# Kernel optimization log

Hardware: AMD Instinct MI355X
Metric: run time of the kernel (lower is better)

## Reference

```python
import jax, jax.numpy as jnp
from jax import lax
import numpy as np

B, T, D, H = 2048, 512, 16, 48


def _lstm_layer(x, W_ih, W_hh, b_ih, b_hh):
    """Single-layer LSTM, batch_first. x: [B,T,Din] -> hs: [B,T,H].
    PyTorch gate order: i, f, g, o."""
    h_dim = W_hh.shape[1]
    # Precompute input contribution for all timesteps: [B,T,4H]
    xg = jnp.einsum('btd,gd->btg', x, W_ih) + b_ih + b_hh
    xg = jnp.swapaxes(xg, 0, 1)  # [T,B,4H]

    def step(carry, xg_t):
        h, c = carry
        gates = xg_t + h @ W_hh.T  # [B,4H]
        i, f, g, o = jnp.split(gates, 4, axis=-1)
        i = jax.nn.sigmoid(i)
        f = jax.nn.sigmoid(f)
        g = jnp.tanh(g)
        o = jax.nn.sigmoid(o)
        c = f * c + i * g
        h = o * jnp.tanh(c)
        return (h, c), h

    bsz = x.shape[0]
    init = (jnp.zeros((bsz, h_dim), x.dtype), jnp.zeros((bsz, h_dim), x.dtype))
    _, hs = lax.scan(step, init, xg)
    return jnp.swapaxes(hs, 0, 1)  # [B,T,H]


def setup_inputs() -> dict:
    key = jax.random.key(0)
    ks = jax.random.split(key, 11)
    s_in = 1.0 / np.sqrt(H)
    return {
        'x': jax.random.normal(ks[0], (B, T, D), jnp.float32),
        'W_ih0': jax.random.normal(ks[1], (4 * H, D), jnp.float32) * s_in,
        'W_hh0': jax.random.normal(ks[2], (4 * H, H), jnp.float32) * s_in,
        'b_ih0': jax.random.normal(ks[3], (4 * H,), jnp.float32) * s_in,
        'b_hh0': jax.random.normal(ks[4], (4 * H,), jnp.float32) * s_in,
        'W_ih1': jax.random.normal(ks[5], (4 * H, H), jnp.float32) * s_in,
        'W_hh1': jax.random.normal(ks[6], (4 * H, H), jnp.float32) * s_in,
        'b_ih1': jax.random.normal(ks[7], (4 * H,), jnp.float32) * s_in,
        'b_hh1': jax.random.normal(ks[8], (4 * H,), jnp.float32) * s_in,
        'fc_w': jax.random.normal(ks[9], (1, H), jnp.float32) * s_in,
        'fc_b': jax.random.normal(ks[10], (1,), jnp.float32) * s_in,
    }


def reference(x, W_ih0, W_hh0, b_ih0, b_hh0, W_ih1, W_hh1, b_ih1, b_hh1, fc_w, fc_b):
    # 2-layer LSTM (eval mode: inter-layer dropout is identity)
    h1 = _lstm_layer(x, W_ih0, W_hh0, b_ih0, b_hh0)   # [B,T,H]
    h2 = _lstm_layer(h1, W_ih1, W_hh1, b_ih1, b_hh1)  # [B,T,H]
    last = h2[:, -1, :]                               # [B,H]
    logits = last @ fc_w.T + fc_b                     # [B,1]
    return jax.nn.sigmoid(logits)
```

## Files before the change

### kernel.cpp

```cpp
#include <hip/hip_runtime.h>

#define TT 512
#define DD 16
#define HH 48
#define BT 8
#define NTHR 768
#define CHUNK 64

#define XB 8192
#define STOT (XB + 1536)

typedef short bf8v __attribute__((ext_vector_type(8)));
typedef float f32x4 __attribute__((ext_vector_type(4)));

__device__ __forceinline__ ushort bfb(float f) {
    return __builtin_bit_cast(ushort, (__bf16)f);
}

__device__ __forceinline__ float sigf(float x) {
    float e = __builtin_amdgcn_exp2f(-1.4426950408889634f * x);
    return __builtin_amdgcn_rcpf(1.0f + e);
}

__device__ __forceinline__ void barrier_lds() {
    asm volatile("s_waitcnt lgkmcnt(0)\ns_barrier" ::: "memory");
}

__global__ __launch_bounds__(NTHR)
void lstm_kernel(const float* __restrict__ x,
                 const float* __restrict__ Wih0, const float* __restrict__ Whh0,
                 const float* __restrict__ bih0, const float* __restrict__ bhh0,
                 const float* __restrict__ Wih1, const float* __restrict__ Whh1,
                 const float* __restrict__ bih1, const float* __restrict__ bhh1,
                 const float* __restrict__ fcw, const float* __restrict__ fcb,
                 float* __restrict__ out)
{
    __shared__ alignas(16) ushort S[STOT];
    __shared__ float outl[BT][HH];

    const int tid  = threadIdx.x;
    const int lane = tid & 63;
    const int wave = tid >> 6;
    const int b0   = blockIdx.x * BT;

    const int colq = lane & 15;
    const int quad = lane >> 4;
    const int b    = colq & 7;
    const bool hi  = (colq >= 8);
    const int u    = wave * 4 + quad;

    const float L2E = 1.4426950408889634f;

    const int fbm = b * 8;
    const bool ringlane = (quad >= 2) && !hi;
    const int r0E = XB + quad * 64 + fbm;
    const int r0O = r0E + 768;
    const int r2E = XB + (8 + quad) * 64 + fbm;
    const int r2O = r2E + 768;
    const int r1statE = XB + (4 + quad) * 64 + fbm;
    const int r1statO = r1statE + 768;
    const int r1ring0 = (quad - 2) * 64 + colq * 8;
    const int inc = ringlane ? 256 : 0;
    const int kk = hi ? 48 + u : u;
    const int woff = (kk >> 3) * 64 + b * 8 + (kk & 7);
    const int wE = XB + 768 + woff;
    const int wO = XB + woff;

    f32x4 bias0, bias1;
#pragma unroll
    for (int r = 0; r < 4; ++r) {
        bias0[r] = bih0[r * 48 + u] + bhh0[r * 48 + u];
        bias1[r] = bih1[r * 48 + u] + bhh1[r * 48 + u];
    }

    const int gi = (colq & 3) * 48 + wave * 4 + (colq >> 2);
    bf8v w0k0, w0k1, w1k0, w1k1, w1k2;
    {
        bf8v w;
#pragma unroll
        for (int j = 0; j < 8; ++j) {
            int k = quad * 8 + j;
            w[j] = (short)bfb(Whh0[gi * 48 + k]);
        }
        w0k0 = w;
#pragma unroll
        for (int j = 0; j < 8; ++j) {
            int k = 32 + quad * 8 + j;
            float v = (k < 48) ? Whh0[gi * 48 + k] : Wih0[gi * 16 + (k - 48)];
            w[j] = (short)bfb(v);
        }
        w0k1 = w;
#pragma unroll
        for (int j = 0; j < 8; ++j) {
            int k = quad * 8 + j;
            w[j] = (short)bfb(Wih1[gi * 48 + k]);
        }
        w1k0 = w;
#pragma unroll
        for (int j = 0; j < 8; ++j) {
            int k = 32 + quad * 8 + j;
            float v = (k < 48) ? Wih1[gi * 48 + k] : Whh1[gi * 48 + (k - 48)];
            w[j] = (short)bfb(v);
        }
        w1k1 = w;
#pragma unroll
        for (int j = 0; j < 8; ++j) {
            int k = 64 + quad * 8 + j;
            w[j] = (short)bfb(Whh1[gi * 48 + (k - 48)]);
        }
        w1k2 = w;
    }

    {
        uint* p = (uint*)S;
        for (int i = tid; i < STOT / 2; i += NTHR) p[i] = 0;
    }
    __syncthreads();

    float c = 0.f;
    float hv = 0.f;

#define MFMA(A, B, C) __builtin_amdgcn_mfma_f32_16x16x32_bf16(A, B, C, 0, 0, 0)

#define BODY(V0A, V1A, V2A, WA, DOL1) { \
        bf8v v0 = *(const bf8v*)&S[V0A]; \
        bf8v v1 = *(const bf8v*)&S[V1A]; \
        bf8v v2 = *(const bf8v*)&S[V2A]; \
        f32x4 acc0 = MFMA(w0k0, v0, bias0); \
        acc0 = MFMA(w0k1, v1, acc0); \
        f32x4 pre; \
        if (DOL1) { \
            f32x4 acc1 = MFMA(w1k0, v0, bias1); \
            acc1 = MFMA(w1k1, v1, acc1); \
            acc1 = MFMA(w1k2, v2, acc1); \
            pre[0] = hi ? acc1[0] : acc0[0]; \
            pre[1] = hi ? acc1[1] : acc0[1]; \
            pre[2] = hi ? acc1[2] : acc0[2]; \
            pre[3] = hi ? acc1[3] : acc0[3]; \
        } else { \
            pre = acc0; \
        } \
        float ei = __builtin_amdgcn_exp2f(-L2E * pre[0]); \
        float ef = __builtin_amdgcn_exp2f(-L2E * pre[1]); \
        float eg = __builtin_amdgcn_exp2f(-2.0f * L2E * pre[2]); \
        float eo = __builtin_amdgcn_exp2f(-L2E * pre[3]); \
        float rig = __builtin_amdgcn_rcpf((1.0f + ei) * (1.0f + eg)); \
        float rf  = __builtin_amdgcn_rcpf(1.0f + ef); \
        float cn = __builtin_fmaf(rf, c, (1.0f - eg) * rig); \
        if (!DOL1) cn = hi ? c : cn;    \
        c = cn; \
        float ec = __builtin_amdgcn_exp2f(-2.0f * L2E * cn); \
        float roc = __builtin_amdgcn_rcpf((1.0f + eo) * (1.0f + ec)); \
        hv = (1.0f - ec) * roc; \
        ushort hb = bfb(hv); \
        if (!hi) { S[WA] = hb; } \
        else if (DOL1) { S[WA] = hb; } \
        barrier_lds(); \
    }

    for (int ck = 0; ck < TT / CHUNK; ++ck) {
        for (int i = tid; i < BT * CHUNK * 4; i += NTHR) {
            int g  = i & 3;
            int tl = (i >> 2) & (CHUNK - 1);
            int bb = i >> 8;
            const float4 v = *(const float4*)(x +
                ((size_t)(b0 + bb) * TT + (ck * CHUNK + tl)) * DD + g * 4);
            ushort4 s4;
            s4.x = bfb(v.x); s4.y = bfb(v.y); s4.z = bfb(v.z); s4.w = bfb(v.w);
            *(ushort4*)&S[tl * 128 + (g >> 1) * 64 + bb * 8 + (g & 1) * 4] = s4;
        }
        __syncthreads();

        int r1E = ringlane ? r1ring0 : r1statE;
        int r1O = ringlane ? (128 + r1ring0) : r1statO;

        int p0 = 0;
        if (ck == 0) {
            BODY(r0E, r1E, r2E, wE, false)
            BODY(r0O, r1O, r2O, wO, true)
            r1E += inc; r1O += inc;
            p0 = 1;
        }
        for (int p = p0; p < CHUNK / 2; ++p) {
            BODY(r0E, r1E, r2E, wE, true)
            BODY(r0O, r1O, r2O, wO, true)
            r1E += inc; r1O += inc;
        }
    }

    {
        int r1E = ringlane ? (r1ring0 + 32 * 256) : r1statE;
        bf8v v0 = *(const bf8v*)&S[r0E];
        bf8v v1 = *(const bf8v*)&S[r1E];
        bf8v v2 = *(const bf8v*)&S[r2E];
        f32x4 acc1 = MFMA(w1k0, v0, bias1);
        acc1 = MFMA(w1k1, v1, acc1);
        acc1 = MFMA(w1k2, v2, acc1);
        float ei = __builtin_amdgcn_exp2f(-L2E * acc1[0]);
        float ef = __builtin_amdgcn_exp2f(-L2E * acc1[1]);
        float eg = __builtin_amdgcn_exp2f(-2.0f * L2E * acc1[2]);
        float eo = __builtin_amdgcn_exp2f(-L2E * acc1[3]);
        float rig = __builtin_amdgcn_rcpf((1.0f + ei) * (1.0f + eg));
        float rf  = __builtin_amdgcn_rcpf(1.0f + ef);
        float cn = __builtin_fmaf(rf, c, (1.0f - eg) * rig);
        float ec = __builtin_amdgcn_exp2f(-2.0f * L2E * cn);
        float roc = __builtin_amdgcn_rcpf((1.0f + eo) * (1.0f + ec));
        hv = (1.0f - ec) * roc;
    }

    if (hi) outl[b][u] = hv;
    __syncthreads();
    if (tid < BT) {
        float s = fcb[0];
        for (int uu = 0; uu < HH; ++uu) s = __builtin_fmaf(outl[tid][uu], fcw[uu], s);
        out[b0 + tid] = sigf(s);
    }
#undef BODY
#undef MFMA
}

extern "C" void kernel_launch(void* const* d_in, const int* in_sizes, int n_in,
                              void* d_out, int out_size, void* d_ws, size_t ws_size,
                              hipStream_t stream) {
    const float* x    = (const float*)d_in[0];
    const float* Wih0 = (const float*)d_in[1];
    const float* Whh0 = (const float*)d_in[2];
    const float* bih0 = (const float*)d_in[3];
    const float* bhh0 = (const float*)d_in[4];
    const float* Wih1 = (const float*)d_in[5];
    const float* Whh1 = (const float*)d_in[6];
    const float* bih1 = (const float*)d_in[7];
    const float* bhh1 = (const float*)d_in[8];
    const float* fcw  = (const float*)d_in[9];
    const float* fcb  = (const float*)d_in[10];
    lstm_kernel<<<2048 / BT, NTHR, 0, stream>>>(x, Wih0, Whh0, bih0, bhh0,
                                                Wih1, Whh1, bih1, bhh1, fcw, fcb,
                                                (float*)d_out);
}
```

Baseline: 287.0 us.

## Halve batch tile to 4 rows, two hidden-unit groups per wave, smaller blocks

Result: slower. 374.0 us (+30.3%).

```diff
diff --git a/kernel.cpp b/kernel.cpp
--- a/kernel.cpp
+++ b/kernel.cpp
@@ -3,12 +3,14 @@
 #define TT 512
 #define DD 16
 #define HH 48
-#define BT 8
-#define NTHR 768
+#define BT 4
+#define NTHR 384
 #define CHUNK 64
-
-#define XB 8192
-#define STOT (XB + 1536)
+#define RS 72
+
+#define XB (CHUNK * RS)
+#define PS 384
+#define STOT (XB + 2 * PS)
 
 typedef short bf8v __attribute__((ext_vector_type(8)));
 typedef float f32x4 __attribute__((ext_vector_type(4)));
@@ -26,7 +28,7 @@
     asm volatile("s_waitcnt lgkmcnt(0)\ns_barrier" ::: "memory");
 }
 
-__global__ __launch_bounds__(NTHR)
+__global__ __launch_bounds__(NTHR, 3)
 void lstm_kernel(const float* __restrict__ x,
                  const float* __restrict__ Wih0, const float* __restrict__ Whh0,
                  const float* __restrict__ bih0, const float* __restrict__ bhh0,
@@ -45,71 +47,82 @@
 
     const int colq = lane & 15;
     const int quad = lane >> 4;
-    const int b    = colq & 7;
-    const bool hi  = (colq >= 8);
-    const int u    = wave * 4 + quad;
+    const int b    = colq & 3;
+    const bool Lb  = ((colq >> 2) & 1) != 0;
+    const bool Tq  = (colq >= 8);
+    const int u    = wave * 8 + (Tq ? 4 : 0) + quad;
 
     const float L2E = 1.4426950408889634f;
 
     const int fbm = b * 8;
-    const bool ringlane = (quad >= 2) && !hi;
-    const int r0E = XB + quad * 64 + fbm;
-    const int r0O = r0E + 768;
-    const int r2E = XB + (8 + quad) * 64 + fbm;
-    const int r2O = r2E + 768;
-    const int r1statE = XB + (4 + quad) * 64 + fbm;
-    const int r1statO = r1statE + 768;
-    const int r1ring0 = (quad - 2) * 64 + colq * 8;
-    const int inc = ringlane ? 256 : 0;
-    const int kk = hi ? 48 + u : u;
-    const int woff = (kk >> 3) * 64 + b * 8 + (kk & 7);
-    const int wE = XB + 768 + woff;
+    const bool ringlane = (quad >= 2) && !Lb;
+    const int r0E = XB + quad * 32 + fbm;
+    const int r0O = r0E + PS;
+    const int r1statE = XB + (4 + quad) * 32 + fbm;
+    const int r1statO = r1statE + PS;
+    const int r2E = XB + (8 + quad) * 32 + fbm;
+    const int r2O = r2E + PS;
+    const int r1ring0 = (quad - 2) * 32 + fbm;
+    const int inc = ringlane ? 2 * RS : 0;
+    const int kk = Lb ? 48 + u : u;
+    const int woff = (kk >> 3) * 32 + fbm + (kk & 7);
+    const int wE = XB + PS + woff;
     const int wO = XB + woff;
 
-    f32x4 bias0, bias1;
+    f32x4 bias00, bias01, bias10, bias11;
+    {
+        const int u0 = wave * 8 + quad;
+        const int u1 = u0 + 4;
 #pragma unroll
-    for (int r = 0; r < 4; ++r) {
-        bias0[r] = bih0[r * 48 + u] + bhh0[r * 48 + u];
-        bias1[r] = bih1[r * 48 + u] + bhh1[r * 48 + u];
-    }
-
-    const int gi = (colq & 3) * 48 + wave * 4 + (colq >> 2);
-    bf8v w0k0, w0k1, w1k0, w1k1, w1k2;
-    {
-        bf8v w;
-#pragma unroll
-        for (int j = 0; j < 8; ++j) {
-            int k = quad * 8 + j;
-            w[j] = (short)bfb(Whh0[gi * 48 + k]);
-        }
-        w0k0 = w;
-#pragma unroll
-        for (int j = 0; j < 8; ++j) {
-            int k = 32 + quad * 8 + j;
-            float v = (k < 48) ? Whh0[gi * 48 + k] : Wih0[gi * 16 + (k - 48)];
-            w[j] = (short)bfb(v);
-        }
-        w0k1 = w;
-#pragma unroll
-        for (int j = 0; j < 8; ++j) {
-            int k = quad * 8 + j;
-            w[j] = (short)bfb(Wih1[gi * 48 + k]);
-        }
-        w1k0 = w;
-#pragma unroll
-        for (int j = 0; j < 8; ++j) {
-            int k = 32 + quad * 8 + j;
-            float v = (k < 48) ? Wih1[gi * 48 + k] : Whh1[gi * 48 + (k - 48)];
-            w[j] = (short)bfb(v);
-        }
-        w1k1 = w;
-#pragma unroll
-        for (int j = 0; j < 8; ++j) {
-            int k = 64 + quad * 8 + j;
-            w[j] = (short)bfb(Whh1[gi * 48 + (k - 48)]);
-        }
-        w1k2 = w;
-    }
+        for (int r = 0; r < 4; ++r) {
+            bias00[r] = bih0[r * 48 + u0] + bhh0[r * 48 + u0];
+            bias01[r] = bih0[r * 48 + u1] + bhh0[r * 48 + u1];
+            bias10[r] = bih1[r * 48 + u0] + bhh1[r * 48 + u0];
+            bias11[r] = bih1[r * 48 + u1] + bhh1[r * 48 + u1];
+        }
+    }
+
+    bf8v w0k0_0, w0k1_0, w1k0_0, w1k1_0, w1k2_0;
+    bf8v w0k0_1, w0k1_1, w1k0_1, w1k1_1, w1k2_1;
+#define LOADW(GI, W0K0, W0K1, W1K0, W1K1, W1K2) { \
+        bf8v w; \
+        _Pragma("unroll") \
+        for (int j = 0; j < 8; ++j) {       \
+            w[j] = (short)bfb(Whh0[(GI) * 48 + quad * 8 + j]); \
+        } \
+        W0K0 = w; \
+        _Pragma("unroll") \
+        for (int j = 0; j < 8; ++j) {       \
+            int k = 32 + quad * 8 + j; \
+            float v = (k < 48) ? Whh0[(GI) * 48 + k] : Wih0[(GI) * 16 + (k - 48)]; \
+            w[j] = (short)bfb(v); \
+        } \
+        W0K1 = w; \
+        _Pragma("unroll") \
+        for (int j = 0; j < 8; ++j) {       \
+            w[j] = (short)bfb(Wih1[(GI) * 48 + quad * 8 + j]); \
+        } \
+        W1K0 = w; \
+        _Pragma("unroll") \
+        for (int j = 0; j < 8; ++j) {       \
+            int k = 32 + quad * 8 + j; \
+            float v = (k < 48) ? Wih1[(GI) * 48 + k] : Whh1[(GI) * 48 + (k - 48)]; \
+            w[j] = (short)bfb(v); \
+        } \
+        W1K1 = w; \
+        _Pragma("unroll") \
+        for (int j = 0; j < 8; ++j) {       \
+            w[j] = (short)bfb(Whh1[(GI) * 48 + 16 + quad * 8 + j]); \
+        } \
+        W1K2 = w; \
+    }
+    {
+        const int gi0 = (colq & 3) * 48 + wave * 8 + (colq >> 2);
+        const int gi1 = gi0 + 4;
+        LOADW(gi0, w0k0_0, w0k1_0, w1k0_0, w1k1_0, w1k2_0)
+        LOADW(gi1, w0k0_1, w0k1_1, w1k0_1, w1k1_1, w1k2_1)
+    }
+#undef LOADW
 
     {
         uint* p = (uint*)S;
@@ -126,19 +139,27 @@
         bf8v v0 = *(const bf8v*)&S[V0A]; \
         bf8v v1 = *(const bf8v*)&S[V1A]; \
         bf8v v2 = *(const bf8v*)&S[V2A]; \
-        f32x4 acc0 = MFMA(w0k0, v0, bias0); \
-        acc0 = MFMA(w0k1, v1, acc0); \
+        f32x4 a00 = MFMA(w0k0_0, v0, bias00); \
+        a00 = MFMA(w0k1_0, v1, a00); \
+        f32x4 a01 = MFMA(w0k0_1, v0, bias01); \
+        a01 = MFMA(w0k1_1, v1, a01); \
         f32x4 pre; \
         if (DOL1) { \
-            f32x4 acc1 = MFMA(w1k0, v0, bias1); \
-            acc1 = MFMA(w1k1, v1, acc1); \
-            acc1 = MFMA(w1k2, v2, acc1); \
-            pre[0] = hi ? acc1[0] : acc0[0]; \
-            pre[1] = hi ? acc1[1] : acc0[1]; \
-            pre[2] = hi ? acc1[2] : acc0[2]; \
-            pre[3] = hi ? acc1[3] : acc0[3]; \
+            f32x4 a10 = MFMA(w1k0_0, v0, bias10); \
+            a10 = MFMA(w1k1_0, v1, a10); \
+            a10 = MFMA(w1k2_0, v2, a10); \
+            f32x4 a11 = MFMA(w1k0_1, v0, bias11); \
+            a11 = MFMA(w1k1_1, v1, a11); \
+            a11 = MFMA(w1k2_1, v2, a11); \
+            _Pragma("unroll") \
+            for (int r = 0; r < 4; ++r) { \
+                float l0 = Tq ? a01[r] : a00[r]; \
+                float l1 = Tq ? a11[r] : a10[r]; \
+                pre[r] = Lb ? l1 : l0; \
+            } \
         } else { \
-            pre = acc0; \
+            _Pragma("unroll") \
+            for (int r = 0; r < 4; ++r) pre[r] = Tq ? a01[r] : a00[r]; \
         } \
         float ei = __builtin_amdgcn_exp2f(-L2E * pre[0]); \
         float ef = __builtin_amdgcn_exp2f(-L2E * pre[1]); \
@@ -147,13 +168,13 @@
         float rig = __builtin_amdgcn_rcpf((1.0f + ei) * (1.0f + eg)); \
         float rf  = __builtin_amdgcn_rcpf(1.0f + ef); \
         float cn = __builtin_fmaf(rf, c, (1.0f - eg) * rig); \
-        if (!DOL1) cn = hi ? c : cn;    \
+        if (!DOL1) cn = Lb ? c : cn;    \
         c = cn; \
         float ec = __builtin_amdgcn_exp2f(-2.0f * L2E * cn); \
         float roc = __builtin_amdgcn_rcpf((1.0f + eo) * (1.0f + ec)); \
         hv = (1.0f - ec) * roc; \
         ushort hb = bfb(hv); \
-        if (!hi) { S[WA] = hb; } \
+        if (!Lb) { S[WA] = hb; } \
         else if (DOL1) { S[WA] = hb; } \
         barrier_lds(); \
     }
@@ -167,12 +188,12 @@
                 ((size_t)(b0 + bb) * TT + (ck * CHUNK + tl)) * DD + g * 4);
             ushort4 s4;
             s4.x = bfb(v.x); s4.y = bfb(v.y); s4.z = bfb(v.z); s4.w = bfb(v.w);
-            *(ushort4*)&S[tl * 128 + (g >> 1) * 64 + bb * 8 + (g & 1) * 4] = s4;
+            *(ushort4*)&S[tl * RS + (g >> 1) * 32 + bb * 8 + (g & 1) * 4] = s4;
         }
         __syncthreads();
 
         int r1E = ringlane ? r1ring0 : r1statE;
-        int r1O = ringlane ? (128 + r1ring0) : r1statO;
+        int r1O = ringlane ? (RS + r1ring0) : r1statO;
 
         int p0 = 0;
         if (ck == 0) {
@@ -189,17 +210,22 @@
     }
 
     {
-        int r1E = ringlane ? (r1ring0 + 32 * 256) : r1statE;
         bf8v v0 = *(const bf8v*)&S[r0E];
-        bf8v v1 = *(const bf8v*)&S[r1E];
+        bf8v v1 = *(const bf8v*)&S[r1statE];
         bf8v v2 = *(const bf8v*)&S[r2E];
-        f32x4 acc1 = MFMA(w1k0, v0, bias1);
-        acc1 = MFMA(w1k1, v1, acc1);
-        acc1 = MFMA(w1k2, v2, acc1);
-        float ei = __builtin_amdgcn_exp2f(-L2E * acc1[0]);
-        float ef = __builtin_amdgcn_exp2f(-L2E * acc1[1]);
-        float eg = __builtin_amdgcn_exp2f(-2.0f * L2E * acc1[2]);
-        float eo = __builtin_amdgcn_exp2f(-L2E * acc1[3]);
+        f32x4 a10 = MFMA(w1k0_0, v0, bias10);
+        a10 = MFMA(w1k1_0, v1, a10);
+        a10 = MFMA(w1k2_0, v2, a10);
+        f32x4 a11 = MFMA(w1k0_1, v0, bias11);
+        a11 = MFMA(w1k1_1, v1, a11);
+        a11 = MFMA(w1k2_1, v2, a11);
+        f32x4 pre;
+#pragma unroll
+        for (int r = 0; r < 4; ++r) pre[r] = Tq ? a11[r] : a10[r];
+        float ei = __builtin_amdgcn_exp2f(-L2E * pre[0]);
+        float ef = __builtin_amdgcn_exp2f(-L2E * pre[1]);
+        float eg = __builtin_amdgcn_exp2f(-2.0f * L2E * pre[2]);
+        float eo = __builtin_amdgcn_exp2f(-L2E * pre[3]);
         float rig = __builtin_amdgcn_rcpf((1.0f + ei) * (1.0f + eg));
         float rf  = __builtin_amdgcn_rcpf(1.0f + ef);
         float cn = __builtin_fmaf(rf, c, (1.0f - eg) * rig);
@@ -208,7 +234,7 @@
         hv = (1.0f - ec) * roc;
     }
 
-    if (hi) outl[b][u] = hv;
+    if (Lb) outl[b][u] = hv;
     __syncthreads();
     if (tid < BT) {
         float s = fcb[0];
```

## Prefetch x chunks into registers, fold exp scales into weights, merge reciprocals

Applied to the files above, without the earlier changes.

Measured after the change: 269.5 us. -6.1%, faster.

```diff
diff --git a/kernel.cpp b/kernel.cpp
--- a/kernel.cpp
+++ b/kernel.cpp
@@ -66,11 +66,14 @@
     const int wE = XB + 768 + woff;
     const int wO = XB + woff;
 
+    const float fac = ((colq & 3) == 2) ? (-2.0f * L2E) : (-L2E);
+
     f32x4 bias0, bias1;
 #pragma unroll
     for (int r = 0; r < 4; ++r) {
-        bias0[r] = bih0[r * 48 + u] + bhh0[r * 48 + u];
-        bias1[r] = bih1[r * 48 + u] + bhh1[r * 48 + u];
+        float fr = (r == 2) ? (-2.0f * L2E) : (-L2E);
+        bias0[r] = fr * (bih0[r * 48 + u] + bhh0[r * 48 + u]);
+        bias1[r] = fr * (bih1[r * 48 + u] + bhh1[r * 48 + u]);
     }
 
     const int gi = (colq & 3) * 48 + wave * 4 + (colq >> 2);
@@ -80,35 +83,58 @@
 #pragma unroll
         for (int j = 0; j < 8; ++j) {
             int k = quad * 8 + j;
-            w[j] = (short)bfb(Whh0[gi * 48 + k]);
+            w[j] = (short)bfb(fac * Whh0[gi * 48 + k]);
         }
         w0k0 = w;
 #pragma unroll
         for (int j = 0; j < 8; ++j) {
             int k = 32 + quad * 8 + j;
             float v = (k < 48) ? Whh0[gi * 48 + k] : Wih0[gi * 16 + (k - 48)];
-            w[j] = (short)bfb(v);
+            w[j] = (short)bfb(fac * v);
         }
         w0k1 = w;
 #pragma unroll
         for (int j = 0; j < 8; ++j) {
             int k = quad * 8 + j;
-            w[j] = (short)bfb(Wih1[gi * 48 + k]);
+            w[j] = (short)bfb(fac * Wih1[gi * 48 + k]);
         }
         w1k0 = w;
 #pragma unroll
         for (int j = 0; j < 8; ++j) {
             int k = 32 + quad * 8 + j;
             float v = (k < 48) ? Wih1[gi * 48 + k] : Whh1[gi * 48 + (k - 48)];
-            w[j] = (short)bfb(v);
+            w[j] = (short)bfb(fac * v);
         }
         w1k1 = w;
 #pragma unroll
         for (int j = 0; j < 8; ++j) {
             int k = 64 + quad * 8 + j;
-            w[j] = (short)bfb(Whh1[gi * 48 + (k - 48)]);
+            w[j] = (short)bfb(fac * Whh1[gi * 48 + (k - 48)]);
         }
         w1k2 = w;
+    }
+
+    const int g_  = tid & 3;
+    const int bb_ = (tid >> 2) & 7;
+    const int tlL = tid >> 5;
+    const float* xpA = x + ((size_t)(b0 + bb_) * TT + tlL) * DD + g_ * 4;
+    const float* xpB = xpA + 24 * DD;
+    const int saA = tlL * 128 + (g_ >> 1) * 64 + bb_ * 8 + (g_ & 1) * 4;
+    const int saB = saA + 24 * 128;
+    float4 st0, st1;
+
+#define STAGE(Hn) { \
+        st0 = *(const float4*)(xpA + (Hn) * (32 * DD)); \
+        if (tid < 256) st1 = *(const float4*)(xpB + (Hn) * (32 * DD)); \
+    }
+#define COMMIT(Hn) { \
+        ushort4 s4; \
+        s4.x = bfb(st0.x); s4.y = bfb(st0.y); s4.z = bfb(st0.z); s4.w = bfb(st0.w); \
+        *(ushort4*)&S[saA + ((Hn) & 1) * 4096] = s4; \
+        if (tid < 256) { \
+            s4.x = bfb(st1.x); s4.y = bfb(st1.y); s4.z = bfb(st1.z); s4.w = bfb(st1.w); \
+            *(ushort4*)&S[saB + ((Hn) & 1) * 4096] = s4; \
+        } \
     }
 
     {
@@ -116,6 +142,11 @@
         for (int i = tid; i < STOT / 2; i += NTHR) p[i] = 0;
     }
     __syncthreads();
+
+    STAGE(0)
+    COMMIT(0)
+    __syncthreads();
+    STAGE(1)
 
     float c = 0.f;
     float hv = 0.f;
@@ -140,13 +171,14 @@
         } else { \
             pre = acc0; \
         } \
-        float ei = __builtin_amdgcn_exp2f(-L2E * pre[0]); \
-        float ef = __builtin_amdgcn_exp2f(-L2E * pre[1]); \
-        float eg = __builtin_amdgcn_exp2f(-2.0f * L2E * pre[2]); \
-        float eo = __builtin_amdgcn_exp2f(-L2E * pre[3]); \
-        float rig = __builtin_amdgcn_rcpf((1.0f + ei) * (1.0f + eg)); \
-        float rf  = __builtin_amdgcn_rcpf(1.0f + ef); \
-        float cn = __builtin_fmaf(rf, c, (1.0f - eg) * rig); \
+        float ei = __builtin_amdgcn_exp2f(pre[0]); \
+        float ef = __builtin_amdgcn_exp2f(pre[1]); \
+        float eg = __builtin_amdgcn_exp2f(pre[2]); \
+        float eo = __builtin_amdgcn_exp2f(pre[3]); \
+        float P = (1.0f + ei) * (1.0f + eg); \
+        float Q = 1.0f + ef; \
+        float R = __builtin_amdgcn_rcpf(P * Q); \
+        float cn = R * __builtin_fmaf(P, c, (1.0f - eg) * Q); \
         if (!DOL1) cn = hi ? c : cn;    \
         c = cn; \
         float ec = __builtin_amdgcn_exp2f(-2.0f * L2E * cn); \
@@ -158,51 +190,47 @@
         barrier_lds(); \
     }
 
-    for (int ck = 0; ck < TT / CHUNK; ++ck) {
-        for (int i = tid; i < BT * CHUNK * 4; i += NTHR) {
-            int g  = i & 3;
-            int tl = (i >> 2) & (CHUNK - 1);
-            int bb = i >> 8;
-            const float4 v = *(const float4*)(x +
-                ((size_t)(b0 + bb) * TT + (ck * CHUNK + tl)) * DD + g * 4);
-            ushort4 s4;
-            s4.x = bfb(v.x); s4.y = bfb(v.y); s4.z = bfb(v.z); s4.w = bfb(v.w);
-            *(ushort4*)&S[tl * 128 + (g >> 1) * 64 + bb * 8 + (g & 1) * 4] = s4;
-        }
-        __syncthreads();
-
-        int r1E = ringlane ? r1ring0 : r1statE;
-        int r1O = ringlane ? (128 + r1ring0) : r1statO;
-
+    int r1E = 0, r1O = 0;
+    for (int H = 0; H < 16; ++H) {
+        if ((H & 1) == 0) {
+            r1E = ringlane ? r1ring0 : r1statE;
+            r1O = ringlane ? (128 + r1ring0) : r1statO;
+        }
         int p0 = 0;
-        if (ck == 0) {
+        if (H == 0) {
             BODY(r0E, r1E, r2E, wE, false)
             BODY(r0O, r1O, r2O, wO, true)
             r1E += inc; r1O += inc;
             p0 = 1;
         }
-        for (int p = p0; p < CHUNK / 2; ++p) {
+        for (int p = p0; p < 16; ++p) {
             BODY(r0E, r1E, r2E, wE, true)
             BODY(r0O, r1O, r2O, wO, true)
             r1E += inc; r1O += inc;
         }
+        if (H < 15) {
+            COMMIT(H + 1)
+            __syncthreads();
+            if (H < 14) STAGE(H + 2)
+        }
     }
 
     {
-        int r1E = ringlane ? (r1ring0 + 32 * 256) : r1statE;
+        int r1p = ringlane ? (r1ring0 + 32 * 256) : r1statE;
         bf8v v0 = *(const bf8v*)&S[r0E];
-        bf8v v1 = *(const bf8v*)&S[r1E];
+        bf8v v1 = *(const bf8v*)&S[r1p];
         bf8v v2 = *(const bf8v*)&S[r2E];
         f32x4 acc1 = MFMA(w1k0, v0, bias1);
         acc1 = MFMA(w1k1, v1, acc1);
         acc1 = MFMA(w1k2, v2, acc1);
-        float ei = __builtin_amdgcn_exp2f(-L2E * acc1[0]);
-        float ef = __builtin_amdgcn_exp2f(-L2E * acc1[1]);
-        float eg = __builtin_amdgcn_exp2f(-2.0f * L2E * acc1[2]);
-        float eo = __builtin_amdgcn_exp2f(-L2E * acc1[3]);
-        float rig = __builtin_amdgcn_rcpf((1.0f + ei) * (1.0f + eg));
-        float rf  = __builtin_amdgcn_rcpf(1.0f + ef);
-        float cn = __builtin_fmaf(rf, c, (1.0f - eg) * rig);
+        float ei = __builtin_amdgcn_exp2f(acc1[0]);
+        float ef = __builtin_amdgcn_exp2f(acc1[1]);
+        float eg = __builtin_amdgcn_exp2f(acc1[2]);
+        float eo = __builtin_amdgcn_exp2f(acc1[3]);
+        float P = (1.0f + ei) * (1.0f + eg);
+        float Q = 1.0f + ef;
+        float R = __builtin_amdgcn_rcpf(P * Q);
+        float cn = R * __builtin_fmaf(P, c, (1.0f - eg) * Q);
         float ec = __builtin_amdgcn_exp2f(-2.0f * L2E * cn);
         float roc = __builtin_amdgcn_rcpf((1.0f + eo) * (1.0f + ec));
         hv = (1.0f - ec) * roc;
@@ -217,6 +245,8 @@
     }
 #undef BODY
 #undef MFMA
+#undef STAGE
+#undef COMMIT
 }
 
 extern "C" void kernel_launch(void* const* d_in, const int* in_sizes, int n_in,
```
